# Kernel tuning notes

Measured on AMD Instinct MI355X. Metric: run time of the kernel, lower is better.

## Reference

```python
import jax, jax.numpy as jnp
import numpy as np

B, S, D, K = 4, 4096, 1024, 64

def setup_inputs() -> dict:
    key = jax.random.key(0)
    kx, kq, kk, kv, ko = jax.random.split(key, 5)
    scale = 1.0 / np.sqrt(D)
    return {
        "x": jax.random.normal(kx, (B, S, D), dtype=jnp.float32),
        "Wq": jax.random.uniform(kq, (K, D), dtype=jnp.float32, minval=-scale, maxval=scale),
        "Wk": jax.random.uniform(kk, (K, D), dtype=jnp.float32, minval=-scale, maxval=scale),
        "Wv": jax.random.uniform(kv, (K, D), dtype=jnp.float32, minval=-scale, maxval=scale),
        "Wo": jax.random.uniform(ko, (D, K), dtype=jnp.float32, minval=-1.0/np.sqrt(K), maxval=1.0/np.sqrt(K)),
    }

def reference(x, Wq, Wk, Wv, Wo):
    # projections: torch Linear(dim, key_dim, bias=False) -> x @ W.T
    Q = jax.nn.elu(x @ Wq.T) + 1.0          # [B,S,K]
    Kf = jax.nn.elu(x @ Wk.T) + 1.0         # [B,S,K]
    V = x @ Wv.T                             # [B,S,K]
    # causal running KV state via cumsum of outer products: [B,S,K,K]
    KV_sum = jnp.cumsum(Kf[..., :, None] * V[..., None, :], axis=1)
    K_sum = jnp.cumsum(Kf, axis=1)           # [B,S,K]
    num = jnp.einsum('bsk,bskm->bsm', Q, KV_sum)   # [B,S,K]
    den = jnp.einsum('bsk,bsk->bs', Q, K_sum)[..., None]
    out = num / (den + 1e-6)
    return out @ Wo.T                         # [B,S,D]
```

## Files before the change

### kernel.cpp

```cpp
#include <hip/hip_runtime.h>

#define BB 4
#define SS 4096
#define DDIM 1024
#define KDIM 64
#define NCHUNK 64
#define TCHUNK 256
#define MROWS 16384

typedef short short8v __attribute__((ext_vector_type(8)));
typedef float f32x4 __attribute__((ext_vector_type(4)));
#define MFMA16 __builtin_amdgcn_mfma_f32_16x16x32_bf16

__device__ __forceinline__ ushort f2bf(float f) {
    uint u = __float_as_uint(f);
    u += 0x7FFFu + ((u >> 16) & 1u);
    return (ushort)(u >> 16);
}

__global__ __launch_bounds__(256) void k_wconv(
    const float* __restrict__ Wq, const float* __restrict__ Wk,
    const float* __restrict__ Wv, const float* __restrict__ Wo,
    ushort* __restrict__ Whf, ushort* __restrict__ Wof)
{
    const int b = blockIdx.x, t = threadIdx.x;
    const int ks = t >> 7;
    const int l = (t >> 1) & 63;
    const int half = t & 1;
    if (b < 192) {
        const int s = b / 12, cf = b % 12;
        const int grow = cf * 16 + (l & 15);
        const int gcol = s * 64 + ks * 32 + ((l >> 4) & 3) * 8 + half * 4;
        const float* src = (grow < 64) ? (Wq + (size_t)grow * DDIM)
                         : (grow < 128) ? (Wk + (size_t)(grow - 64) * DDIM)
                                        : (Wv + (size_t)(grow - 128) * DDIM);
        float4 v = *(const float4*)&src[gcol];
        ushort* dst = &Whf[(size_t)(((s * 12 + cf) * 2 + ks) * 64 + l) * 8 + half * 4];
        dst[0] = f2bf(v.x); dst[1] = f2bf(v.y); dst[2] = f2bf(v.z); dst[3] = f2bf(v.w);
    } else {
        const int cf = b - 192;
        const int d = cf * 16 + (l & 15);
        const int kc = ks * 32 + ((l >> 4) & 3) * 8 + half * 4;
        float4 v = *(const float4*)&Wo[(size_t)d * KDIM + kc];
        ushort* dst = &Wof[(size_t)((cf * 2 + ks) * 64 + l) * 8 + half * 4];
        dst[0] = f2bf(v.x); dst[1] = f2bf(v.y); dst[2] = f2bf(v.z); dst[3] = f2bf(v.w);
    }
}

#define EBP 216
__global__ __launch_bounds__(256) void k_proj(
    const float* __restrict__ x, const ushort* __restrict__ Whf,
    ushort* __restrict__ Qf, ushort* __restrict__ Kff,
    ushort* __restrict__ KfT, ushort* __restrict__ VT)
{
    __shared__ ushort xs[64 * 512];
    const int t = threadIdx.x;
    const int w = t >> 6, l = t & 63;
    const int mb = blockIdx.x;
    const int row0 = mb * 32;

    {
        const int r = t & 31;
        const int kb = (t >> 5) * 128;
        const int rf = r >> 4, rl = r & 15;
        const float* xrow = &x[(size_t)(row0 + r) * DDIM + kb];
#pragma unroll
        for (int kc = 0; kc < 128; kc += 8) {
            float4 u0 = *(const float4*)(xrow + kc);
            float4 u1 = *(const float4*)(xrow + kc + 4);
            short8v h;
            h[0] = (short)f2bf(u0.x); h[1] = (short)f2bf(u0.y);
            h[2] = (short)f2bf(u0.z); h[3] = (short)f2bf(u0.w);
            h[4] = (short)f2bf(u1.x); h[5] = (short)f2bf(u1.y);
            h[6] = (short)f2bf(u1.z); h[7] = (short)f2bf(u1.w);
            const int k = kb + kc;
            const int frag = rf * 32 + (k >> 5);
            const int lane = rl | (((k >> 3) & 3) << 4);
            *(short8v*)&xs[(size_t)(frag * 64 + lane) * 8] = h;
        }
    }
    __syncthreads();

    f32x4 acc[2][3];
#pragma unroll
    for (int r = 0; r < 2; ++r)
#pragma unroll
        for (int c = 0; c < 3; ++c) acc[r][c] = (f32x4){0.f, 0.f, 0.f, 0.f};

    auto loadW = [&](int s, short8v (&bw)[6]) {
#pragma unroll
        for (int j = 0; j < 6; ++j) {
            const int cf = w * 3 + (j >> 1);
            const int f = cf * 2 + (j & 1);
            bw[j] = *(const short8v*)&Whf[((size_t)(s * 24 + f)) * 512 + l * 8];
        }
    };
    auto computeStep = [&](int s, short8v (&bw)[6]) {
#pragma unroll
        for (int ks = 0; ks < 2; ++ks) {
            const int kk = s * 2 + ks;
            short8v a0 = *(const short8v*)&xs[(size_t)((kk) * 64 + l) * 8];
            short8v a1 = *(const short8v*)&xs[(size_t)((32 + kk) * 64 + l) * 8];
#pragma unroll
            for (int c = 0; c < 3; ++c) {
                acc[0][c] = MFMA16(a0, bw[c * 2 + ks], acc[0][c], 0, 0, 0);
                acc[1][c] = MFMA16(a1, bw[c * 2 + ks], acc[1][c], 0, 0, 0);
            }
        }
    };

    short8v bwA[6], bwB[6];
    loadW(0, bwA);
    for (int s = 0; s < 16; s += 2) {
        loadW(s + 1, bwB);
        computeStep(s, bwA);
        if (s + 2 < 16) loadW(s + 2, bwA);
        computeStep(s + 1, bwB);
    }

    __syncthreads();
    ushort* eb = xs;
#pragma unroll
    for (int rf = 0; rf < 2; ++rf)
#pragma unroll
        for (int c = 0; c < 3; ++c) {
            const int col = w * 48 + c * 16 + (l & 15);
#pragma unroll
            for (int q = 0; q < 4; ++q) {
                const int rl = rf * 16 + ((l >> 4) << 2) + q;
                float v = acc[rf][c][q];
                if (col < 128) v = (v > 0.f) ? v + 1.f : __expf(v);
                eb[rl * EBP + col] = f2bf(v);
            }
        }
    __syncthreads();

    {
        const int rf = t >> 7, ks = (t >> 6) & 1, lam = t & 63;
        const int r = rf * 16 + (lam & 15);
        const int c0 = ks * 32 + ((lam >> 4) & 3) * 8;
        short8v q8 = *(const short8v*)&eb[r * EBP + c0];
        short8v k8 = *(const short8v*)&eb[r * EBP + 64 + c0];
        const size_t fo = ((size_t)(mb * 4 + rf * 2 + ks)) * 512 + lam * 8;
        *(short8v*)&Qf[fo] = q8;
        *(short8v*)&Kff[fo] = k8;
    }
    {
        const int f = t >> 6, lam = t & 63;
        const int kcol = 64 + f * 16 + (lam & 15);
        const int vcol = 128 + f * 16 + (lam & 15);
        const int jb = ((lam >> 4) & 3) * 8;
        short8v kT, vT;
#pragma unroll
        for (int e = 0; e < 8; ++e) {
            kT[e] = (short)eb[(jb + e) * EBP + kcol];
            vT[e] = (short)eb[(jb + e) * EBP + vcol];
        }
        const size_t fo = ((size_t)((mb >> 1) * 8 + f * 2 + (mb & 1))) * 512 + lam * 8;
        *(short8v*)&KfT[fo] = kT;
        *(short8v*)&VT[fo] = vT;
    }
}

__global__ __launch_bounds__(64) void k_chunksum(
    const ushort* __restrict__ KfT, const ushort* __restrict__ VT,
    float* __restrict__ KVc, float* __restrict__ Ksc)
{
    const int g = blockIdx.x, l = threadIdx.x;
    short8v ka[4][2], vb[4][2];
#pragma unroll
    for (int f = 0; f < 4; ++f)
#pragma unroll
        for (int js = 0; js < 2; ++js) {
            const size_t fo = ((size_t)(g * 8 + f * 2 + js)) * 512 + l * 8;
            ka[f][js] = *(const short8v*)&KfT[fo];
            vb[f][js] = *(const short8v*)&VT[fo];
        }
    short8v onesf;
#pragma unroll
    for (int e = 0; e < 8; ++e) onesf[e] = ((l & 15) == 0) ? (short)0x3F80 : (short)0;

    f32x4 acc[4][5];
#pragma unroll
    for (int kf = 0; kf < 4; ++kf)
#pragma unroll
        for (int mf = 0; mf < 5; ++mf) acc[kf][mf] = (f32x4){0.f, 0.f, 0.f, 0.f};
#pragma unroll
    for (int js = 0; js < 2; ++js)
#pragma unroll
        for (int kf = 0; kf < 4; ++kf) {
#pragma unroll
            for (int mf = 0; mf < 4; ++mf)
                acc[kf][mf] = MFMA16(ka[kf][js], vb[mf][js], acc[kf][mf], 0, 0, 0);
            acc[kf][4] = MFMA16(ka[kf][js], onesf, acc[kf][4], 0, 0, 0);
        }
    const int lq = l >> 4;
#pragma unroll
    for (int kf = 0; kf < 4; ++kf) {
#pragma unroll
        for (int q = 0; q < 4; ++q) {
            const int k = kf * 16 + lq * 4 + q;
#pragma unroll
            for (int mf = 0; mf < 4; ++mf)
                KVc[(size_t)g * 4096 + k * 64 + mf * 16 + (l & 15)] = acc[kf][mf][q];
            if ((l & 15) == 0) Ksc[(size_t)g * KDIM + k] = acc[kf][4][q];
        }
    }
}

__global__ void k_scan(const float* __restrict__ KVc, const float* __restrict__ Ksc,
                       float* __restrict__ Sst, float* __restrict__ Kss)
{
    const int b = blockIdx.x / 65;
    const int r = blockIdx.x % 65;
    const int t = threadIdx.x;
    float acc = 0.f;
    if (r < 64) {
        const int e = r * 64 + t;
        for (int c0 = 0; c0 < NCHUNK; c0 += 8) {
            float v[8];
#pragma unroll
            for (int i = 0; i < 8; ++i)
                v[i] = KVc[((size_t)(b * NCHUNK + c0 + i)) * 4096 + e];
#pragma unroll
            for (int i = 0; i < 8; ++i) {
                Sst[((size_t)(b * NCHUNK + c0 + i)) * 4096 + e] = acc;
                acc += v[i];
            }
        }
    } else {
        for (int c0 = 0; c0 < NCHUNK; c0 += 8) {
            float v[8];
#pragma unroll
            for (int i = 0; i < 8; ++i)
                v[i] = Ksc[((size_t)(b * NCHUNK + c0 + i)) * KDIM + t];
#pragma unroll
            for (int i = 0; i < 8; ++i) {
                Kss[((size_t)(b * NCHUNK + c0 + i)) * KDIM + t] = acc;
                acc += v[i];
            }
        }
    }
}

__global__ __launch_bounds__(256) void k_intra(
    const ushort* __restrict__ Qf, const ushort* __restrict__ Kff,
    const ushort* __restrict__ VT, const float* __restrict__ Sst,
    const float* __restrict__ Kss, const ushort* __restrict__ Wof,
    float* __restrict__ out)
{
    __shared__ ushort pb[64 * 64];
    __shared__ ushort sT[80 * 64];
    const int g = blockIdx.x, t = threadIdx.x;
    const int w = t >> 6, l = t & 63;
    const int lq = l >> 4;

    {
        const int k = t >> 2, m0 = (t & 3) * 16;
        const float4* sp = (const float4*)&Sst[(size_t)g * 4096 + k * 64 + m0];
        float4 f0 = sp[0], f1 = sp[1], f2v = sp[2], f3 = sp[3];
        float fv[16] = {f0.x, f0.y, f0.z, f0.w, f1.x, f1.y, f1.z, f1.w,
                        f2v.x, f2v.y, f2v.z, f2v.w, f3.x, f3.y, f3.z, f3.w};
#pragma unroll
        for (int i = 0; i < 16; ++i) {
            const int m = m0 + i;
            sT[m * 64 + (k ^ ((m & 7) << 3))] = f2bf(fv[i]);
        }
        if (t < 64) sT[64 * 64 + t] = f2bf(Kss[(size_t)g * KDIM + t]);
        for (int idx = t; idx < 960; idx += 256) sT[65 * 64 + idx] = 0;
    }

    short8v qa[2], kb[4][2];
    {
        const int mb = g * 2 + (w >> 1), rf = w & 1;
#pragma unroll
        for (int ks = 0; ks < 2; ++ks)
            qa[ks] = *(const short8v*)&Qf[((size_t)(mb * 4 + rf * 2 + ks)) * 512 + l * 8];
#pragma unroll
        for (int cf = 0; cf < 4; ++cf)
#pragma unroll
            for (int ks = 0; ks < 2; ++ks)
                kb[cf][ks] = *(const short8v*)&Kff[((size_t)((g * 2 + (cf >> 1)) * 4 + (cf & 1) * 2 + ks)) * 512 + l * 8];
    }
    f32x4 accs[4];
#pragma unroll
    for (int cf = 0; cf < 4; ++cf) accs[cf] = (f32x4){0.f, 0.f, 0.f, 0.f};
#pragma unroll
    for (int ks = 0; ks < 2; ++ks)
#pragma unroll
        for (int cf = 0; cf < 4; ++cf)
            accs[cf] = MFMA16(qa[ks], kb[cf][ks], accs[cf], 0, 0, 0);
#pragma unroll
    for (int cf = 0; cf < 4; ++cf)
#pragma unroll
        for (int q = 0; q < 4; ++q) {
            const int row = w * 16 + lq * 4 + q;
            const int col = cf * 16 + (l & 15);
            const float sv = (col <= row) ? accs[cf][q] : 0.f;
            pb[row * 64 + (col ^ ((row & 7) << 3))] = f2bf(sv);
        }
    __syncthreads();

    f32x4 accn[5];
#pragma unroll
    for (int mf = 0; mf < 5; ++mf) accn[mf] = (f32x4){0.f, 0.f, 0.f, 0.f};
    short8v onesf;
#pragma unroll
    for (int e = 0; e < 8; ++e) onesf[e] = ((l & 15) == 0) ? (short)0x3F80 : (short)0;
#pragma unroll
    for (int js = 0; js < 2; ++js) {
        const int prow = w * 16 + (l & 15);
        const int pbase = js * 32 + ((l >> 4) & 3) * 8;
        short8v pa = *(const short8v*)&pb[prow * 64 + (pbase ^ ((prow & 7) << 3))];
#pragma unroll
        for (int mf = 0; mf < 4; ++mf) {
            short8v vb = *(const short8v*)&VT[((size_t)(g * 8 + mf * 2 + js)) * 512 + l * 8];
            accn[mf] = MFMA16(pa, vb, accn[mf], 0, 0, 0);
        }
        accn[4] = MFMA16(pa, onesf, accn[4], 0, 0, 0);
    }
#pragma unroll
    for (int ks = 0; ks < 2; ++ks) {
        const int base = ks * 32 + ((l >> 4) & 3) * 8;
#pragma unroll
        for (int mf = 0; mf < 5; ++mf) {
            const int row = mf * 16 + (l & 15);
            short8v sb = *(const short8v*)&sT[row * 64 + (base ^ ((row & 7) << 3))];
            accn[mf] = MFMA16(qa[ks], sb, accn[mf], 0, 0, 0);
        }
    }
#pragma unroll
    for (int q = 0; q < 4; ++q) {
        const float den = __shfl(accn[4][q], (l & 48));
        const float rinv = 1.f / (den + 1e-6f);
        const int row = w * 16 + lq * 4 + q;
#pragma unroll
        for (int mf = 0; mf < 4; ++mf) {
            const int col = mf * 16 + (l & 15);
            pb[row * 64 + (col ^ ((row & 7) << 3))] = f2bf(accn[mf][q] * rinv);
        }
    }
    __syncthreads();

    short8v oa[4][2];
#pragma unroll
    for (int rf = 0; rf < 4; ++rf)
#pragma unroll
        for (int ks = 0; ks < 2; ++ks) {
            const int row = rf * 16 + (l & 15);
            const int base = ks * 32 + ((l >> 4) & 3) * 8;
            oa[rf][ks] = *(const short8v*)&pb[row * 64 + (base ^ ((row & 7) << 3))];
        }
#pragma unroll
    for (int rr = 0; rr < 4; ++rr) {
        f32x4 acco[4][4];
#pragma unroll
        for (int rf = 0; rf < 4; ++rf)
#pragma unroll
            for (int ci = 0; ci < 4; ++ci) acco[rf][ci] = (f32x4){0.f, 0.f, 0.f, 0.f};
#pragma unroll
        for (int ci = 0; ci < 4; ++ci) {
            const int cfg = w * 16 + rr * 4 + ci;
#pragma unroll
            for (int ks = 0; ks < 2; ++ks) {
                short8v wb = *(const short8v*)&Wof[((size_t)(cfg * 2 + ks)) * 512 + l * 8];
#pragma unroll
                for (int rf = 0; rf < 4; ++rf)
                    acco[rf][ci] = MFMA16(oa[rf][ks], wb, acco[rf][ci], 0, 0, 0);
            }
        }
#pragma unroll
        for (int rf = 0; rf < 4; ++rf)
#pragma unroll
            for (int ci = 0; ci < 4; ++ci)
#pragma unroll
                for (int q = 0; q < 4; ++q)
                    out[((size_t)(g * 64 + rf * 16 + lq * 4 + q)) * DDIM
                        + w * 256 + rr * 64 + ci * 16 + (l & 15)] = acco[rf][ci][q];
    }
}

extern "C" void kernel_launch(void* const* d_in, const int* in_sizes, int n_in,
                              void* d_out, int out_size, void* d_ws, size_t ws_size,
                              hipStream_t stream)
{
    const float* x  = (const float*)d_in[0];
    const float* Wq = (const float*)d_in[1];
    const float* Wk = (const float*)d_in[2];
    const float* Wv = (const float*)d_in[3];
    const float* Wo = (const float*)d_in[4];
    float* out = (float*)d_out;

    float* ws   = (float*)d_ws;
    float* KVc  = ws;
    float* Sst  = KVc + (size_t)TCHUNK * 4096;
    float* Ksc  = Sst + (size_t)TCHUNK * 4096;
    float* Kss  = Ksc + (size_t)TCHUNK * KDIM;
    ushort* Whf = (ushort*)(Kss + (size_t)TCHUNK * KDIM);
    ushort* Wof = Whf + (size_t)192 * DDIM;
    ushort* Qf  = Wof + (size_t)64 * 1024;
    ushort* Kff = Qf  + (size_t)512 * 4 * 512;
    ushort* KfT = Kff + (size_t)512 * 4 * 512;
    ushort* VT  = KfT + (size_t)256 * 8 * 512;

    k_wconv<<<dim3(256), dim3(256), 0, stream>>>(Wq, Wk, Wv, Wo, Whf, Wof);
    k_proj<<<dim3(MROWS / 32), dim3(256), 0, stream>>>(x, Whf, Qf, Kff, KfT, VT);
    k_chunksum<<<dim3(TCHUNK), dim3(64), 0, stream>>>(KfT, VT, KVc, Ksc);
    k_scan<<<dim3(BB * 65), dim3(64), 0, stream>>>(KVc, Ksc, Sst, Kss);
    k_intra<<<dim3(TCHUNK), dim3(256), 0, stream>>>(Qf, Kff, VT, Sst, Kss, Wof, out);
}
```

Before: 64.07 us.

## Halve projection LDS staging, fully unroll scan loads, vectorize output stores via LDS

The projection kernel now stages x in two 512-column halves with an XOR-swizzled LDS layout, which halves shared memory per block so more blocks can be resident and bank conflicts drop. The scan kernel loads all 64 chunk values up front before the serial prefix sum, exposing more memory-level parallelism at the cost of more registers. The intra kernel writes output tiles through a per-wave LDS buffer so it can issue float4 coalesced global stores instead of scattered scalar ones. This adds an extra barrier in projection and extra LDS traffic in the output path.

```diff
diff --git a/kernel.cpp b/kernel.cpp
--- a/kernel.cpp
+++ b/kernel.cpp
@@ -53,54 +53,52 @@
     ushort* __restrict__ Qf, ushort* __restrict__ Kff,
     ushort* __restrict__ KfT, ushort* __restrict__ VT)
 {
-    __shared__ ushort xs[64 * 512];
+    __shared__ ushort xs[32 * 512];
     const int t = threadIdx.x;
     const int w = t >> 6, l = t & 63;
     const int mb = blockIdx.x;
     const int row0 = mb * 32;
 
-    {
-        const int r = t & 31;
-        const int kb = (t >> 5) * 128;
-        const int rf = r >> 4, rl = r & 15;
-        const float* xrow = &x[(size_t)(row0 + r) * DDIM + kb];
-#pragma unroll
-        for (int kc = 0; kc < 128; kc += 8) {
-            float4 u0 = *(const float4*)(xrow + kc);
-            float4 u1 = *(const float4*)(xrow + kc + 4);
-            short8v h;
-            h[0] = (short)f2bf(u0.x); h[1] = (short)f2bf(u0.y);
-            h[2] = (short)f2bf(u0.z); h[3] = (short)f2bf(u0.w);
-            h[4] = (short)f2bf(u1.x); h[5] = (short)f2bf(u1.y);
-            h[6] = (short)f2bf(u1.z); h[7] = (short)f2bf(u1.w);
-            const int k = kb + kc;
-            const int frag = rf * 32 + (k >> 5);
-            const int lane = rl | (((k >> 3) & 3) << 4);
-            *(short8v*)&xs[(size_t)(frag * 64 + lane) * 8] = h;
-        }
-    }
-    __syncthreads();
-
     f32x4 acc[2][3];
 #pragma unroll
     for (int r = 0; r < 2; ++r)
 #pragma unroll
         for (int c = 0; c < 3; ++c) acc[r][c] = (f32x4){0.f, 0.f, 0.f, 0.f};
 
-    auto loadW = [&](int s, short8v (&bw)[6]) {
+    auto stageX = [&](int h) {
+#pragma unroll
+        for (int i = 0; i < 8; ++i) {
+            const int fidx = i * 256 + t;
+            const int r = fidx >> 6;
+            const int c = (fidx & 63) * 8;
+            const float* p = &x[(size_t)(row0 + r) * DDIM + h * 512 + c];
+            float4 u0 = *(const float4*)p;
+            float4 u1 = *(const float4*)(p + 4);
+            short8v hh;
+            hh[0] = (short)f2bf(u0.x); hh[1] = (short)f2bf(u0.y);
+            hh[2] = (short)f2bf(u0.z); hh[3] = (short)f2bf(u0.w);
+            hh[4] = (short)f2bf(u1.x); hh[5] = (short)f2bf(u1.y);
+            hh[6] = (short)f2bf(u1.z); hh[7] = (short)f2bf(u1.w);
+            const int frag = (r >> 4) * 16 + (c >> 5);
+            const int slot = ((r & 15) | (((c >> 3) & 3) << 4)) ^ (frag & 7);
+            *(short8v*)&xs[(size_t)(frag * 64 + slot) * 8] = hh;
+        }
+    };
+    auto loadW = [&](int sg, short8v (&bw)[6]) {
 #pragma unroll
         for (int j = 0; j < 6; ++j) {
             const int cf = w * 3 + (j >> 1);
             const int f = cf * 2 + (j & 1);
-            bw[j] = *(const short8v*)&Whf[((size_t)(s * 24 + f)) * 512 + l * 8];
+            bw[j] = *(const short8v*)&Whf[((size_t)(sg * 24 + f)) * 512 + l * 8];
         }
     };
-    auto computeStep = [&](int s, short8v (&bw)[6]) {
+    auto computeStep = [&](int sl, short8v (&bw)[6]) {
 #pragma unroll
         for (int ks = 0; ks < 2; ++ks) {
-            const int kk = s * 2 + ks;
-            short8v a0 = *(const short8v*)&xs[(size_t)((kk) * 64 + l) * 8];
-            short8v a1 = *(const short8v*)&xs[(size_t)((32 + kk) * 64 + l) * 8];
+            const int kkl = sl * 2 + ks;
+            const int f0 = kkl, f1 = 16 + kkl;
+            short8v a0 = *(const short8v*)&xs[(size_t)(f0 * 64 + (l ^ (f0 & 7))) * 8];
+            short8v a1 = *(const short8v*)&xs[(size_t)(f1 * 64 + (l ^ (f1 & 7))) * 8];
 #pragma unroll
             for (int c = 0; c < 3; ++c) {
                 acc[0][c] = MFMA16(a0, bw[c * 2 + ks], acc[0][c], 0, 0, 0);
@@ -109,13 +107,18 @@
         }
     };
 
-    short8v bwA[6], bwB[6];
-    loadW(0, bwA);
-    for (int s = 0; s < 16; s += 2) {
-        loadW(s + 1, bwB);
-        computeStep(s, bwA);
-        if (s + 2 < 16) loadW(s + 2, bwA);
-        computeStep(s + 1, bwB);
+    for (int h = 0; h < 2; ++h) {
+        if (h) __syncthreads();
+        stageX(h);
+        __syncthreads();
+        short8v bwA[6], bwB[6];
+        loadW(h * 8, bwA);
+        for (int s = 0; s < 8; s += 2) {
+            loadW(h * 8 + s + 1, bwB);
+            computeStep(s, bwA);
+            if (s + 2 < 8) loadW(h * 8 + s + 2, bwA);
+            computeStep(s + 1, bwB);
+        }
     }
 
     __syncthreads();
@@ -214,31 +217,28 @@
     const int b = blockIdx.x / 65;
     const int r = blockIdx.x % 65;
     const int t = threadIdx.x;
-    float acc = 0.f;
     if (r < 64) {
         const int e = r * 64 + t;
-        for (int c0 = 0; c0 < NCHUNK; c0 += 8) {
-            float v[8];
-#pragma unroll
-            for (int i = 0; i < 8; ++i)
-                v[i] = KVc[((size_t)(b * NCHUNK + c0 + i)) * 4096 + e];
-#pragma unroll
-            for (int i = 0; i < 8; ++i) {
-                Sst[((size_t)(b * NCHUNK + c0 + i)) * 4096 + e] = acc;
-                acc += v[i];
-            }
+        float v[64];
+#pragma unroll
+        for (int i = 0; i < 64; ++i)
+            v[i] = KVc[((size_t)(b * NCHUNK + i)) * 4096 + e];
+        float acc = 0.f;
+#pragma unroll
+        for (int i = 0; i < 64; ++i) {
+            Sst[((size_t)(b * NCHUNK + i)) * 4096 + e] = acc;
+            acc += v[i];
         }
     } else {
-        for (int c0 = 0; c0 < NCHUNK; c0 += 8) {
-            float v[8];
-#pragma unroll
-            for (int i = 0; i < 8; ++i)
-                v[i] = Ksc[((size_t)(b * NCHUNK + c0 + i)) * KDIM + t];
-#pragma unroll
-            for (int i = 0; i < 8; ++i) {
-                Kss[((size_t)(b * NCHUNK + c0 + i)) * KDIM + t] = acc;
-                acc += v[i];
-            }
+        float v[64];
+#pragma unroll
+        for (int i = 0; i < 64; ++i)
+            v[i] = Ksc[((size_t)(b * NCHUNK + i)) * KDIM + t];
+        float acc = 0.f;
+#pragma unroll
+        for (int i = 0; i < 64; ++i) {
+            Kss[((size_t)(b * NCHUNK + i)) * KDIM + t] = acc;
+            acc += v[i];
         }
     }
 }
@@ -251,6 +251,7 @@
 {
     __shared__ ushort pb[64 * 64];
     __shared__ ushort sT[80 * 64];
+    __shared__ float ob[4][16 * 68 + 4];
     const int g = blockIdx.x, t = threadIdx.x;
     const int w = t >> 6, l = t & 63;
     const int lq = l >> 4;
@@ -351,6 +352,7 @@
             const int base = ks * 32 + ((l >> 4) & 3) * 8;
             oa[rf][ks] = *(const short8v*)&pb[row * 64 + (base ^ ((row & 7) << 3))];
         }
+    float* obw = ob[w];
 #pragma unroll
     for (int rr = 0; rr < 4; ++rr) {
         f32x4 acco[4][4];
@@ -370,13 +372,20 @@
             }
         }
 #pragma unroll
-        for (int rf = 0; rf < 4; ++rf)
+        for (int rf = 0; rf < 4; ++rf) {
 #pragma unroll
             for (int ci = 0; ci < 4; ++ci)
 #pragma unroll
                 for (int q = 0; q < 4; ++q)
-                    out[((size_t)(g * 64 + rf * 16 + lq * 4 + q)) * DDIM
-                        + w * 256 + rr * 64 + ci * 16 + (l & 15)] = acco[rf][ci][q];
+                    obw[(lq * 4 + q) * 68 + ci * 16 + (l & 15)] = acco[rf][ci][q];
+#pragma unroll
+            for (int rg = 0; rg < 4; ++rg) {
+                const int row = rg * 4 + lq;
+                float4 vv = *(const float4*)&obw[row * 68 + (l & 15) * 4];
+                *(float4*)&out[((size_t)(g * 64 + rf * 16 + row)) * DDIM
+                               + w * 256 + rr * 64 + (l & 15) * 4] = vv;
+            }
+        }
     }
 }
 
```

Measured after the change: 58.01 us. 1.1x faster.
